# Kernel tuning notes

Hardware: AMD Instinct MI355X
Metric: run time of the kernel (lower is better)

The kernel has to match this reference:

```python
import jax, jax.numpy as jnp
import numpy as np

H = 12
D_K = 64
NEG = -1e9
EPS = 1e-6
SQRT_2_PI = float(np.sqrt(2.0 / np.pi))


def gelu_tanh(x):
    return 0.5 * x * (1.0 + jnp.tanh(SQRT_2_PI * (x + 0.044715 * x * x * x)))


def layernorm(x, a, b):
    # torch std is unbiased (ddof=1); note original adds eps to std, not var
    mean = jnp.mean(x, axis=-1, keepdims=True)
    n = x.shape[-1]
    var = jnp.sum((x - mean) ** 2, axis=-1, keepdims=True) / (n - 1)
    std = jnp.sqrt(var)
    return a * (x - mean) / (std + EPS) + b


def setup_inputs() -> dict:
    key = jax.random.key(0)
    ks = jax.random.split(key, 16)
    B, S, D, F = 8, 1024, 768, 3072
    s = 0.02
    inp = {
        "x": jax.random.normal(ks[0], (B, S, D), jnp.float32),
        "mask": jnp.ones((B, 1, 1, S), jnp.int32),
        "Wq": jax.random.normal(ks[1], (D, D), jnp.float32) * s,
        "bq": jnp.zeros((D,), jnp.float32),
        "Wk": jax.random.normal(ks[2], (D, D), jnp.float32) * s,
        "bk": jnp.zeros((D,), jnp.float32),
        "Wv": jax.random.normal(ks[3], (D, D), jnp.float32) * s,
        "bv": jnp.zeros((D,), jnp.float32),
        "Wo": jax.random.normal(ks[4], (D, D), jnp.float32) * s,
        "bo": jnp.zeros((D,), jnp.float32),
        "W1": jax.random.normal(ks[5], (D, F), jnp.float32) * s,
        "b1": jnp.zeros((F,), jnp.float32),
        "W2": jax.random.normal(ks[6], (F, D), jnp.float32) * s,
        "b2": jnp.zeros((D,), jnp.float32),
        "ln1_a": jnp.ones((D,), jnp.float32),
        "ln1_b": jnp.ones((D,), jnp.float32),
        "ln2_a": jnp.ones((D,), jnp.float32),
        "ln2_b": jnp.ones((D,), jnp.float32),
    }
    return inp


def reference(x, mask, Wq, bq, Wk, bk, Wv, bv, Wo, bo, W1, b1, W2, b2,
              ln1_a, ln1_b, ln2_a, ln2_b):
    B, S, D = x.shape
    # QKV projections -> [B, H, S, d_k]
    def split_heads(t):
        return t.reshape(B, S, H, D_K).transpose(0, 2, 1, 3)
    q = split_heads(x @ Wq + bq)
    k = split_heads(x @ Wk + bk)
    v = split_heads(x @ Wv + bv)
    scores = jnp.einsum("bhqd,bhkd->bhqk", q, k) / jnp.sqrt(jnp.float32(D_K))
    scores = jnp.where(mask == 0, jnp.float32(NEG), scores)
    p = jax.nn.softmax(scores, axis=-1)
    attn = jnp.einsum("bhqk,bhkd->bhqd", p, v)
    attn = attn.transpose(0, 2, 1, 3).reshape(B, S, D)
    attn_out = attn @ Wo + bo
    out1 = layernorm(x + attn_out, ln1_a, ln1_b)
    ffn = gelu_tanh(out1 @ W1 + b1) @ W2 + b2
    out2 = layernorm(out1 + ffn, ln2_a, ln2_b)
    return out2
```

## Files before the change

kernel.cpp:

```cpp
#include <hip/hip_runtime.h>
#include <hip/hip_bf16.h>
#include <math.h>

#define BB 8
#define SS 1024
#define DD 768
#define FF 3072
#define HH 12
#define DK 64

typedef __bf16 bf16;
typedef __attribute__((ext_vector_type(8))) __bf16 bf16x8;
typedef __attribute__((ext_vector_type(4))) __bf16 bf16x4;
typedef __attribute__((ext_vector_type(4))) float f32x4;

#define AS1 __attribute__((address_space(1)))
#define AS3 __attribute__((address_space(3)))

#define EXP2_SCALE 0.18033688011112042f
#define NLOG2E2    -2.8853900817779268f
#define MASK_BIAS  -1.8033688e8f

__device__ __forceinline__ float gelu_fast(float x) {
    const float u = 0.7978845608028654f * (x + 0.044715f * x * x * x);
    const float e = __builtin_amdgcn_exp2f(u * NLOG2E2);
    return x * __builtin_amdgcn_rcpf(1.0f + e);
}

template<int BN, int OUTB, int GELU_F, int RESID>
__global__ __launch_bounds__(256) void gemm_bf16(
    const bf16* __restrict__ A, const bf16* __restrict__ Bt,
    const float* __restrict__ bias, const float* __restrict__ R,
    void* __restrict__ Cout, int M, int N, int K)
{
    constexpr int NTJ   = BN / 32;
    constexpr int BITER = (BN * 8) / 256;

    __shared__ bf16x8 As[1024];
    __shared__ bf16x8 Bs[BN * 8];

    const int t    = threadIdx.x;
    const int wave = t >> 6;
    const int lane = t & 63;
    const int mtiles = M >> 7;
    const int m0 = (blockIdx.x % mtiles) * 128;
    const int n0 = (blockIdx.x / mtiles) * BN;
    const int wm = (wave >> 1) * 64;
    const int wn = (wave & 1) * (BN / 2);
    const int col  = lane & 15;
    const int quad = lane >> 4;

    f32x4 acc[4][NTJ] = {};

    const bf16* Abase = A  + (size_t)m0 * K;
    const bf16* Bbase = Bt + (size_t)n0 * K;

    for (int k0 = 0; k0 < K; k0 += 64) {
        if (k0) __syncthreads();

        #pragma unroll
        for (int i = 0; i < 4; ++i) {
            const int chunk = i * 256 + wave * 64 + lane;
            const int r  = chunk >> 3;
            const int kc = (chunk & 7) ^ (r & 7);
            const bf16* ga = Abase + (size_t)r * K + k0 + kc * 8;
            __builtin_amdgcn_global_load_lds((AS1 void*)ga, (AS3 void*)(As + i * 256 + wave * 64), 16, 0, 0);
        }
        #pragma unroll
        for (int i = 0; i < BITER; ++i) {
            const int chunk = i * 256 + wave * 64 + lane;
            const int r  = chunk >> 3;
            const int kc = (chunk & 7) ^ (r & 7);
            const bf16* gb = Bbase + (size_t)r * K + k0 + kc * 8;
            __builtin_amdgcn_global_load_lds((AS1 void*)gb, (AS3 void*)(Bs + i * 256 + wave * 64), 16, 0, 0);
        }
        __syncthreads();

        const bf16* Asp = (const bf16*)As;
        const bf16* Bsp = (const bf16*)Bs;
        #pragma unroll
        for (int ks = 0; ks < 2; ++ks) {
            bf16x8 af[4], bfr[NTJ];
            #pragma unroll
            for (int ti = 0; ti < 4; ++ti) {
                const int r  = wm + ti * 16 + col;
                const int cs = (ks * 4 + quad) ^ (r & 7);
                af[ti] = *(const bf16x8*)(Asp + r * 64 + cs * 8);
            }
            #pragma unroll
            for (int tj = 0; tj < NTJ; ++tj) {
                const int r  = wn + tj * 16 + col;
                const int cs = (ks * 4 + quad) ^ (r & 7);
                bfr[tj] = *(const bf16x8*)(Bsp + r * 64 + cs * 8);
            }
            #pragma unroll
            for (int ti = 0; ti < 4; ++ti)
                #pragma unroll
                for (int tj = 0; tj < NTJ; ++tj)
                    acc[ti][tj] = __builtin_amdgcn_mfma_f32_16x16x32_bf16(
                        af[ti], bfr[tj], acc[ti][tj], 0, 0, 0);
        }
    }

    float biasv[NTJ];
    #pragma unroll
    for (int tj = 0; tj < NTJ; ++tj) biasv[tj] = bias[n0 + wn + tj * 16 + col];

    #pragma unroll
    for (int ti = 0; ti < 4; ++ti) {
        #pragma unroll
        for (int tj = 0; tj < NTJ; ++tj) {
            const int n = n0 + wn + tj * 16 + col;
            #pragma unroll
            for (int i = 0; i < 4; ++i) {
                const int m = m0 + wm + ti * 16 + quad * 4 + i;
                float v = acc[ti][tj][i] + biasv[tj];
                if (GELU_F) v = gelu_fast(v);
                if (RESID) v += R[(size_t)m * N + n];
                if (OUTB) ((bf16*)Cout)[(size_t)m * N + n] = (bf16)v;
                else      ((float*)Cout)[(size_t)m * N + n] = v;
            }
        }
    }
}

__device__ __forceinline__ void tc32(
    const float* __restrict__ src, bf16* __restrict__ dst,
    int R, int C, int c0, int r0, int t)
{
    __shared__ float tile[32][33];
    const int tx = t & 31, ty = t >> 5;
    #pragma unroll
    for (int i = 0; i < 32; i += 8)
        tile[ty + i][tx] = src[(size_t)(r0 + ty + i) * C + c0 + tx];
    __syncthreads();
    #pragma unroll
    for (int i = 0; i < 32; i += 8)
        dst[(size_t)(c0 + ty + i) * R + r0 + tx] = (bf16)tile[tx][ty + i];
}

__global__ __launch_bounds__(256) void prep_all(
    const float* __restrict__ Wq, const float* __restrict__ Wk,
    const float* __restrict__ Wv, const float* __restrict__ Wo,
    const float* __restrict__ W1, const float* __restrict__ W2,
    const float* __restrict__ bq, const float* __restrict__ bk,
    const float* __restrict__ bv, const float* __restrict__ x,
    bf16* __restrict__ wqkvb, bf16* __restrict__ wob,
    bf16* __restrict__ wt1b,  bf16* __restrict__ wt2b,
    float* __restrict__ bqkv, bf16x4* __restrict__ xb)
{
    const int blk = blockIdx.x;
    const int t = threadIdx.x;
    if (blk < 2304) {
        const int job = blk / 576, loc = blk % 576;
        const int c0 = (loc % 24) * 32, r0 = (loc / 24) * 32;
        const float* src = (job == 0) ? Wq : (job == 1) ? Wk : (job == 2) ? Wv : Wo;
        bf16* dst = (job == 3) ? wob : wqkvb + (size_t)job * DD * DD;
        tc32(src, dst, DD, DD, c0, r0, t);
    } else if (blk < 4608) {
        const int loc = blk - 2304;
        tc32(W1, wt1b, DD, FF, (loc % 96) * 32, (loc / 96) * 32, t);
    } else if (blk < 6912) {
        const int loc = blk - 4608;
        tc32(W2, wt2b, FF, DD, (loc % 24) * 32, (loc / 24) * 32, t);
    } else if (blk < 6921) {
        const int i = (blk - 6912) * 256 + t;
        if (i < 3 * DD)
            bqkv[i] = (i < DD) ? bq[i] : (i < 2 * DD ? bk[i - DD] : bv[i - 2 * DD]);
    } else {
        const int i = (blk - 6921) * 256 + t;
        const float4 v = ((const float4*)x)[i];
        bf16x4 o;
        o.x = (bf16)v.x; o.y = (bf16)v.y; o.z = (bf16)v.z; o.w = (bf16)v.w;
        xb[i] = o;
    }
}

__global__ __launch_bounds__(256) void vtrans(
    const bf16* __restrict__ qkvb, bf16* __restrict__ vtb)
{
    __shared__ bf16 tile[32][33];
    const int s0 = blockIdx.x * 32, d0 = blockIdx.y * 32;
    const int bh = blockIdx.z;
    const int b = bh / HH, h = bh % HH;
    const int tx = threadIdx.x & 31, ty = threadIdx.x >> 5;
    #pragma unroll
    for (int i = 0; i < 32; i += 8)
        tile[ty + i][tx] = qkvb[(size_t)(b * SS + s0 + ty + i) * 2304 + 1536 + h * DK + d0 + tx];
    __syncthreads();
    #pragma unroll
    for (int i = 0; i < 32; i += 8)
        vtb[(size_t)(bh * DK + d0 + ty + i) * SS + s0 + tx] = tile[tx][ty + i];
}

__global__ __launch_bounds__(256) void flash_mfma(
    const bf16* __restrict__ qkvb,
    const bf16* __restrict__ vtb,
    const int*  __restrict__ mask,
    bf16* __restrict__ O)
{
    __shared__ bf16  Ps[4 * 32 * 64];
    __shared__ float Mb[SS];

    const int t    = threadIdx.x;
    const int wave = t >> 6;
    const int lane = t & 63;
    const int col  = lane & 15;
    const int quad = lane >> 4;
    const int bh = blockIdx.x % (BB * HH);
    const int q0 = (blockIdx.x / (BB * HH)) * 128;
    const int b  = bh / HH;
    const int h  = bh % HH;

    #pragma unroll
    for (int i = 0; i < 4; ++i) {
        const int c = t + i * 256;
        Mb[c] = (mask[b * SS + c] == 0) ? MASK_BIAS : 0.0f;
    }

    bf16x8 aq[2][2];
    #pragma unroll
    for (int mi = 0; mi < 2; ++mi)
        #pragma unroll
        for (int ks = 0; ks < 2; ++ks)
            aq[mi][ks] = *(const bf16x8*)(qkvb
                + (size_t)(b * SS + q0 + wave * 32 + mi * 16 + col) * 2304
                + h * DK + ks * 32 + quad * 8);

    __syncthreads();

    const bf16* Kg = qkvb + (size_t)b * SS * 2304 + DD + h * DK;
    const bf16* Vg = vtb + (size_t)bh * DK * SS;

    f32x4 o[2][4] = {};
    float l_part[2][4] = {};
    bf16* Pw = Ps + wave * 2048;

    for (int it = 0; it < SS / 64; ++it) {
        const int c0 = it * 64;

        bf16x8 kf[2][4];
        #pragma unroll
        for (int ks = 0; ks < 2; ++ks)
            #pragma unroll
            for (int tj = 0; tj < 4; ++tj)
                kf[ks][tj] = *(const bf16x8*)(Kg
                    + (size_t)(c0 + tj * 16 + col) * 2304 + ks * 32 + quad * 8);

        f32x4 s4[2][4] = {};
        #pragma unroll
        for (int mi = 0; mi < 2; ++mi)
            #pragma unroll
            for (int ks = 0; ks < 2; ++ks)
                #pragma unroll
                for (int tj = 0; tj < 4; ++tj)
                    s4[mi][tj] = __builtin_amdgcn_mfma_f32_16x16x32_bf16(
                        aq[mi][ks], kf[ks][tj], s4[mi][tj], 0, 0, 0);

        bf16x8 vf[2][4];
        #pragma unroll
        for (int ks = 0; ks < 2; ++ks)
            #pragma unroll
            for (int tj = 0; tj < 4; ++tj)
                vf[ks][tj] = *(const bf16x8*)(Vg
                    + (size_t)(tj * 16 + col) * SS + c0 + ks * 32 + quad * 8);

        float mbv[4];
        #pragma unroll
        for (int tj = 0; tj < 4; ++tj) mbv[tj] = Mb[c0 + tj * 16 + col];

        #pragma unroll
        for (int mi = 0; mi < 2; ++mi)
            #pragma unroll
            for (int i = 0; i < 4; ++i) {
                const int rf = mi * 16 + quad * 4 + i;
                #pragma unroll
                for (int tj = 0; tj < 4; ++tj) {
                    const float p = __builtin_amdgcn_exp2f(
                        __builtin_fmaf(s4[mi][tj][i], EXP2_SCALE, mbv[tj]));
                    l_part[mi][i] += p;
                    const int c  = tj * 16 + col;
                    const int sl = ((c >> 3) ^ (rf & 7));
                    Pw[rf * 64 + sl * 8 + (c & 7)] = (bf16)p;
                }
            }

        #pragma unroll
        for (int mi = 0; mi < 2; ++mi) {
            bf16x8 pf[2];
            #pragma unroll
            for (int ks = 0; ks < 2; ++ks) {
                const int rf = mi * 16 + col;
                const int sl = (ks * 4 + quad) ^ (rf & 7);
                pf[ks] = *(const bf16x8*)(Pw + rf * 64 + sl * 8);
            }
            #pragma unroll
            for (int ks = 0; ks < 2; ++ks)
                #pragma unroll
                for (int tj = 0; tj < 4; ++tj)
                    o[mi][tj] = __builtin_amdgcn_mfma_f32_16x16x32_bf16(
                        pf[ks], vf[ks][tj], o[mi][tj], 0, 0, 0);
        }
    }

    #pragma unroll
    for (int mi = 0; mi < 2; ++mi)
        #pragma unroll
        for (int i = 0; i < 4; ++i) {
            float l = l_part[mi][i];
            #pragma unroll
            for (int off = 1; off < 16; off <<= 1)
                l += __shfl_xor(l, off, 64);
            const float inv = 1.0f / l;
            const int q = q0 + wave * 32 + mi * 16 + quad * 4 + i;
            #pragma unroll
            for (int tj = 0; tj < 4; ++tj)
                O[(size_t)(b * SS + q) * DD + h * DK + tj * 16 + col] =
                    (bf16)(o[mi][tj][i] * inv);
        }
}

__global__ __launch_bounds__(256) void layernorm_k(
    const float* __restrict__ X,
    const float* __restrict__ ga, const float* __restrict__ gb,
    float* __restrict__ out, bf16* __restrict__ outb)
{
    __shared__ float red[4];
    const int row = blockIdx.x;
    const int t   = threadIdx.x;
    const float* x = X + (size_t)row * DD;

    float v[3];
    #pragma unroll
    for (int i = 0; i < 3; ++i) v[i] = x[t + i * 256];

    float s = v[0] + v[1] + v[2];
    #pragma unroll
    for (int off = 32; off > 0; off >>= 1) s += __shfl_down(s, off, 64);
    if ((t & 63) == 0) red[t >> 6] = s;
    __syncthreads();
    const float mean = (red[0] + red[1] + red[2] + red[3]) * (1.0f / 768.0f);
    __syncthreads();

    float sq = 0.f;
    #pragma unroll
    for (int i = 0; i < 3; ++i) { const float d = v[i] - mean; sq += d * d; }
    #pragma unroll
    for (int off = 32; off > 0; off >>= 1) sq += __shfl_down(sq, off, 64);
    if ((t & 63) == 0) red[t >> 6] = sq;
    __syncthreads();
    const float var = (red[0] + red[1] + red[2] + red[3]) * (1.0f / 767.0f);
    const float inv = 1.0f / (sqrtf(var) + 1e-6f);

    #pragma unroll
    for (int i = 0; i < 3; ++i) {
        const int c = t + i * 256;
        const float r = ga[c] * (v[i] - mean) * inv + gb[c];
        out[(size_t)row * DD + c] = r;
        if (outb) outb[(size_t)row * DD + c] = (bf16)r;
    }
}

extern "C" void kernel_launch(void* const* d_in, const int* in_sizes, int n_in,
                              void* d_out, int out_size, void* d_ws, size_t ws_size,
                              hipStream_t stream)
{
    const float* x    = (const float*)d_in[0];
    const int*   mask = (const int*)  d_in[1];
    const float* Wq   = (const float*)d_in[2];
    const float* bq   = (const float*)d_in[3];
    const float* Wk   = (const float*)d_in[4];
    const float* bk   = (const float*)d_in[5];
    const float* Wv   = (const float*)d_in[6];
    const float* bv   = (const float*)d_in[7];
    const float* Wo   = (const float*)d_in[8];
    const float* bo   = (const float*)d_in[9];
    const float* W1   = (const float*)d_in[10];
    const float* b1   = (const float*)d_in[11];
    const float* W2   = (const float*)d_in[12];
    const float* b2   = (const float*)d_in[13];
    const float* ln1a = (const float*)d_in[14];
    const float* ln1b = (const float*)d_in[15];
    const float* ln2a = (const float*)d_in[16];
    const float* ln2b = (const float*)d_in[17];
    float* out = (float*)d_out;

    const int M = BB * SS;
    const size_t nBSD = (size_t)M * DD;

    char* w = (char*)d_ws;
    bf16*  qkvb  = (bf16*)w;            w += (size_t)M * 3 * DD * 2;
    bf16*  vtb   = (bf16*)w;            w += (size_t)BB * HH * DK * SS * 2;
    bf16*  attnb = (bf16*)w;            w += nBSD * 2;
    float* attn_sum = (float*)w;        w += nBSD * 4;
    float* out1  = (float*)w;           w += nBSD * 4;
    float* ffn_sum = (float*)w;         w += nBSD * 4;
    bf16*  xb    = (bf16*)w;            w += nBSD * 2;
    bf16*  hbuf  = (bf16*)w;            w += (size_t)M * FF * 2;
    bf16*  wqkvb = (bf16*)w;            w += (size_t)3 * DD * DD * 2;
    bf16*  wob   = (bf16*)w;            w += (size_t)DD * DD * 2;
    bf16*  wt1b  = (bf16*)w;            w += (size_t)DD * FF * 2;
    bf16*  wt2b  = (bf16*)w;            w += (size_t)FF * DD * 2;
    float* bqkv  = (float*)w;           w += (size_t)3 * DD * 4;
    bf16*  out1b = xb;

    const dim3 blk(256);

    prep_all<<<dim3(13065), blk, 0, stream>>>(
        Wq, Wk, Wv, Wo, W1, W2, bq, bk, bv, x,
        wqkvb, wob, wt1b, wt2b, bqkv, (bf16x4*)xb);

    gemm_bf16<128, 1, 0, 0><<<dim3((M / 128) * (3 * DD / 128)), blk, 0, stream>>>(
        xb, wqkvb, bqkv, nullptr, qkvb, M, 3 * DD, DD);

    vtrans<<<dim3(SS / 32, DK / 32, BB * HH), blk, 0, stream>>>(qkvb, vtb);

    flash_mfma<<<dim3((SS / 128) * BB * HH), blk, 0, stream>>>(qkvb, vtb, mask, attnb);

    gemm_bf16<64, 0, 0, 1><<<dim3((M / 128) * (DD / 64)), blk, 0, stream>>>(
        attnb, wob, bo, x, attn_sum, M, DD, DD);

    layernorm_k<<<dim3(M), blk, 0, stream>>>(attn_sum, ln1a, ln1b, out1, out1b);

    gemm_bf16<128, 1, 1, 0><<<dim3((M / 128) * (FF / 128)), blk, 0, stream>>>(
        out1b, wt1b, b1, nullptr, hbuf, M, FF, DD);

    gemm_bf16<64, 0, 0, 1><<<dim3((M / 128) * (DD / 64)), blk, 0, stream>>>(
        hbuf, wt2b, b2, out1, ffn_sum, M, DD, FF);

    layernorm_k<<<dim3(M), blk, 0, stream>>>(ffn_sum, ln2a, ln2b, out, nullptr);
}
```

Before: 407.3 us.

## Stage K and V tiles in LDS via direct global-to-LDS loads in flash attention

The flash attention kernel now copies 128-key blocks of K and V^T into shared memory with swizzled global_load_lds, so all four waves share one copy. Previously each wave read its own K and V fragments straight from global memory. Each staged block is processed as two 64-key sub-steps read from LDS. This cuts redundant global and L2 traffic across waves, at the cost of a block-wide barrier per tile with no double buffering and more LDS use, which may lower occupancy.

New measurement: 364.0 us. 1.12x faster.

```diff
diff --git a/kernel.cpp b/kernel.cpp
--- a/kernel.cpp
+++ b/kernel.cpp
@@ -199,8 +199,10 @@
     const int*  __restrict__ mask,
     bf16* __restrict__ O)
 {
-    __shared__ bf16  Ps[4 * 32 * 64];
-    __shared__ float Mb[SS];
+    __shared__ bf16x8 Ks[1024];
+    __shared__ bf16x8 Vs[1024];
+    __shared__ bf16   Ps[4 * 32 * 64];
+    __shared__ float  Mb[SS];
 
     const int t    = threadIdx.x;
     const int wave = t >> 6;
@@ -227,79 +229,108 @@
                 + (size_t)(b * SS + q0 + wave * 32 + mi * 16 + col) * 2304
                 + h * DK + ks * 32 + quad * 8);
 
-    __syncthreads();
-
-    const bf16* Kg = qkvb + (size_t)b * SS * 2304 + DD + h * DK;
-    const bf16* Vg = vtb + (size_t)bh * DK * SS;
-
     f32x4 o[2][4] = {};
     float l_part[2][4] = {};
     bf16* Pw = Ps + wave * 2048;
 
-    for (int it = 0; it < SS / 64; ++it) {
-        const int c0 = it * 64;
-
-        bf16x8 kf[2][4];
-        #pragma unroll
-        for (int ks = 0; ks < 2; ++ks)
-            #pragma unroll
-            for (int tj = 0; tj < 4; ++tj)
-                kf[ks][tj] = *(const bf16x8*)(Kg
-                    + (size_t)(c0 + tj * 16 + col) * 2304 + ks * 32 + quad * 8);
-
-        f32x4 s4[2][4] = {};
-        #pragma unroll
-        for (int mi = 0; mi < 2; ++mi)
+    for (int it = 0; it < SS / 128; ++it) {
+        const int c0 = it * 128;
+        if (it) __syncthreads();
+
+        #pragma unroll
+        for (int i = 0; i < 4; ++i) {
+            const int chunk = i * 256 + wave * 64 + lane;
+            const int r  = chunk >> 3;
+            const int kc = (chunk & 7) ^ (r & 7);
+            const bf16* gk = qkvb + (size_t)(b * SS + c0 + r) * 2304 + DD + h * DK + kc * 8;
+            __builtin_amdgcn_global_load_lds((AS1 void*)gk,
+                (AS3 void*)(Ks + i * 256 + wave * 64), 16, 0, 0);
+        }
+        #pragma unroll
+        for (int i = 0; i < 4; ++i) {
+            const int chunk = i * 256 + wave * 64 + lane;
+            const int r  = chunk >> 4;
+            const int cc = (chunk & 15) ^ (r & 15);
+            const bf16* gv = vtb + (size_t)(bh * DK + r) * SS + c0 + cc * 8;
+            __builtin_amdgcn_global_load_lds((AS1 void*)gv,
+                (AS3 void*)(Vs + i * 256 + wave * 64), 16, 0, 0);
+        }
+        __syncthreads();
+
+        const bf16* Ksp = (const bf16*)Ks;
+        const bf16* Vsp = (const bf16*)Vs;
+
+        #pragma unroll
+        for (int ss = 0; ss < 2; ++ss) {
+            const int cb = c0 + ss * 64;
+
+            bf16x8 kf[2][4];
             #pragma unroll
             for (int ks = 0; ks < 2; ++ks)
                 #pragma unroll
-                for (int tj = 0; tj < 4; ++tj)
-                    s4[mi][tj] = __builtin_amdgcn_mfma_f32_16x16x32_bf16(
-                        aq[mi][ks], kf[ks][tj], s4[mi][tj], 0, 0, 0);
-
-        bf16x8 vf[2][4];
-        #pragma unroll
-        for (int ks = 0; ks < 2; ++ks)
-            #pragma unroll
-            for (int tj = 0; tj < 4; ++tj)
-                vf[ks][tj] = *(const bf16x8*)(Vg
-                    + (size_t)(tj * 16 + col) * SS + c0 + ks * 32 + quad * 8);
-
-        float mbv[4];
-        #pragma unroll
-        for (int tj = 0; tj < 4; ++tj) mbv[tj] = Mb[c0 + tj * 16 + col];
-
-        #pragma unroll
-        for (int mi = 0; mi < 2; ++mi)
-            #pragma unroll
-            for (int i = 0; i < 4; ++i) {
-                const int rf = mi * 16 + quad * 4 + i;
-                #pragma unroll
                 for (int tj = 0; tj < 4; ++tj) {
-                    const float p = __builtin_amdgcn_exp2f(
-                        __builtin_fmaf(s4[mi][tj][i], EXP2_SCALE, mbv[tj]));
-                    l_part[mi][i] += p;
-                    const int c  = tj * 16 + col;
-                    const int sl = ((c >> 3) ^ (rf & 7));
-                    Pw[rf * 64 + sl * 8 + (c & 7)] = (bf16)p;
+                    const int r  = ss * 64 + tj * 16 + col;
+                    const int sl = (ks * 4 + quad) ^ (r & 7);
+                    kf[ks][tj] = *(const bf16x8*)(Ksp + r * 64 + sl * 8);
                 }
+
+            f32x4 s4[2][4] = {};
+            #pragma unroll
+            for (int mi = 0; mi < 2; ++mi)
+                #pragma unroll
+                for (int ks = 0; ks < 2; ++ks)
+                    #pragma unroll
+                    for (int tj = 0; tj < 4; ++tj)
+                        s4[mi][tj] = __builtin_amdgcn_mfma_f32_16x16x32_bf16(
+                            aq[mi][ks], kf[ks][tj], s4[mi][tj], 0, 0, 0);
+
+            bf16x8 vf[2][4];
+            #pragma unroll
+            for (int ks = 0; ks < 2; ++ks)
+                #pragma unroll
+                for (int tj = 0; tj < 4; ++tj) {
+                    const int r  = tj * 16 + col;
+                    const int lc = ss * 8 + ks * 4 + quad;
+                    const int sl = lc ^ (r & 15);
+                    vf[ks][tj] = *(const bf16x8*)(Vsp + r * 128 + sl * 8);
+                }
+
+            float mbv[4];
+            #pragma unroll
+            for (int tj = 0; tj < 4; ++tj) mbv[tj] = Mb[cb + tj * 16 + col];
+
+            #pragma unroll
+            for (int mi = 0; mi < 2; ++mi)
+                #pragma unroll
+                for (int i = 0; i < 4; ++i) {
+                    const int rf = mi * 16 + quad * 4 + i;
+                    #pragma unroll
+                    for (int tj = 0; tj < 4; ++tj) {
+                        const float p = __builtin_amdgcn_exp2f(
+                            __builtin_fmaf(s4[mi][tj][i], EXP2_SCALE, mbv[tj]));
+                        l_part[mi][i] += p;
+                        const int c  = tj * 16 + col;
+                        const int sl = ((c >> 3) ^ (rf & 7));
+                        Pw[rf * 64 + sl * 8 + (c & 7)] = (bf16)p;
+                    }
+                }
+
+            #pragma unroll
+            for (int mi = 0; mi < 2; ++mi) {
+                bf16x8 pf[2];
+                #pragma unroll
+                for (int ks = 0; ks < 2; ++ks) {
+                    const int rf = mi * 16 + col;
+                    const int sl = (ks * 4 + quad) ^ (rf & 7);
+                    pf[ks] = *(const bf16x8*)(Pw + rf * 64 + sl * 8);
+                }
+                #pragma unroll
+                for (int ks = 0; ks < 2; ++ks)
+                    #pragma unroll
+                    for (int tj = 0; tj < 4; ++tj)
+                        o[mi][tj] = __builtin_amdgcn_mfma_f32_16x16x32_bf16(
+                            pf[ks], vf[ks][tj], o[mi][tj], 0, 0, 0);
             }
-
-        #pragma unroll
-        for (int mi = 0; mi < 2; ++mi) {
-            bf16x8 pf[2];
-            #pragma unroll
-            for (int ks = 0; ks < 2; ++ks) {
-                const int rf = mi * 16 + col;
-                const int sl = (ks * 4 + quad) ^ (rf & 7);
-                pf[ks] = *(const bf16x8*)(Pw + rf * 64 + sl * 8);
-            }
-            #pragma unroll
-            for (int ks = 0; ks < 2; ++ks)
-                #pragma unroll
-                for (int tj = 0; tj < 4; ++tj)
-                    o[mi][tj] = __builtin_amdgcn_mfma_f32_16x16x32_bf16(
-                        pf[ks], vf[ks][tj], o[mi][tj], 0, 0, 0);
         }
     }
 
```
